# Kernel tuning notes

Measured on AMD Instinct MI355X. Metric: run time of the kernel, lower is better.

The kernel has to match this reference:

```python
import jax, jax.numpy as jnp
import numpy as np

PI_2 = 3.14159 / 2  # matches torch module constant (not exact pi/2, keeps tan finite)
EPS_SUM = 1e-07
EPS_COS = 1e-08  # torch F.cosine_similarity default eps


def setup_inputs() -> dict:
    key = jax.random.key(0)
    k1, k2 = jax.random.split(key)
    B, N, C, H, W = 16, 2000, 512, 7, 7
    # memory is uniform-initialized then sum-normalized per cube, as in __init__
    memory = jax.random.uniform(k1, (N, C, H, W), dtype=jnp.float32)
    memory = memory / (jnp.sum(memory, axis=(1, 2, 3), keepdims=True) + EPS_SUM)
    key_t = jax.random.uniform(k2, (B, C, H, W), dtype=jnp.float32)
    return {"key": key_t, "memory": memory}


def reference(key, memory):
    # _normalize: divide key by its per-sample sum
    k = key / (jnp.sum(key, axis=(1, 2, 3), keepdims=True) + EPS_SUM)
    B = k.shape[0]
    N = memory.shape[0]
    kf = k.reshape(B, -1)            # [B, D], D = C*H*W
    mf = memory.reshape(N, -1)       # [N, D]
    # cosine similarity (torch clamps each norm to eps)
    dots = jnp.einsum('bd,nd->bn', kf, mf)                       # [B, N]
    kn = jnp.maximum(jnp.linalg.norm(kf, axis=-1), EPS_COS)      # [B]
    mn = jnp.maximum(jnp.linalg.norm(mf, axis=-1), EPS_COS)      # [N]
    cos = dots / (kn[:, None] * mn[None, :])
    w = jax.nn.softmax(jnp.tan(cos * PI_2), axis=1)              # [B, N]
    # read: sum over memory cubes weighted by address w
    return jnp.einsum('bn,nchw->bchw', w, memory)                # [B, C, H, W]
```

## Files before the change

kernel.cpp:

```cpp
#include <hip/hip_runtime.h>
#include <math.h>

#define B 16
#define N 2000
#define D 25088
#define D4 6272
#define PI2 1.570795f
#define KC 28
#define KSPAN (D / KC)
#define KTILES (KSPAN / 32)
#define NT (D / 32)
#define NCHUNK 20
#define NPER (N / NCHUNK)
#define SELHI 0x07060302u

typedef __attribute__((ext_vector_type(8))) short short8;
typedef __attribute__((ext_vector_type(4))) float f32x4;
typedef unsigned int uint;

union pk { uint4 u; short8 s; };
__device__ __forceinline__ short8 as_s8(uint4 u) { pk p; p.u = u; return p.s; }

__device__ __forceinline__ float wave_sum(float v) {
#pragma unroll
    for (int off = 32; off > 0; off >>= 1) v += __shfl_xor(v, off, 64);
    return v;
}
__device__ __forceinline__ float wave_max(float v) {
#pragma unroll
    for (int off = 32; off > 0; off >>= 1) v = fmaxf(v, __shfl_xor(v, off, 64));
    return v;
}

__device__ __forceinline__ void cvt_hilo(const float4& a, const float4& b,
                                         short8& hi, short8& lo, float4& msqv) {
    float xs[8] = {a.x, a.y, a.z, a.w, b.x, b.y, b.z, b.w};
    float* mq = &msqv.x;
    uint lu[8];
#pragma unroll
    for (int j = 0; j < 8; ++j) {
        uint u = __float_as_uint(xs[j]);
        float lof = xs[j] - __uint_as_float(u & 0xffff0000u);
        lu[j] = __float_as_uint(lof);
        mq[j & 3] = fmaf(xs[j], xs[j], mq[j & 3]);
    }
    uint4 h, l;
    h.x = __builtin_amdgcn_perm(__float_as_uint(xs[1]), __float_as_uint(xs[0]), SELHI);
    h.y = __builtin_amdgcn_perm(__float_as_uint(xs[3]), __float_as_uint(xs[2]), SELHI);
    h.z = __builtin_amdgcn_perm(__float_as_uint(xs[5]), __float_as_uint(xs[4]), SELHI);
    h.w = __builtin_amdgcn_perm(__float_as_uint(xs[7]), __float_as_uint(xs[6]), SELHI);
    l.x = __builtin_amdgcn_perm(lu[1], lu[0], SELHI);
    l.y = __builtin_amdgcn_perm(lu[3], lu[2], SELHI);
    l.z = __builtin_amdgcn_perm(lu[5], lu[4], SELHI);
    l.w = __builtin_amdgcn_perm(lu[7], lu[6], SELHI);
    hi = as_s8(h); lo = as_s8(l);
}

__global__ void k_split(const float* __restrict__ key, unsigned short* __restrict__ ksw,
                        float* __restrict__ kn2) {
    const int tid  = threadIdx.x;
    const int g    = blockIdx.x * 256 + tid;
    const int tile = g >> 6, lane = g & 63;
    const int m = lane & 15, quad = lane >> 4;
    const float* src = key + (size_t)m * D + tile * 32 + quad * 8;
    float4 x0 = *(const float4*)src;
    float4 x1 = *(const float4*)(src + 4);
    short8 hi, lo;
    float4 msqv = {0.f, 0.f, 0.f, 0.f};
    cvt_hilo(x0, x1, hi, lo, msqv);
    pk ph; ph.s = hi;
    pk pl; pl.s = lo;
    *(uint4*)(ksw + ((size_t)tile * 64 + lane) * 8)        = ph.u;
    *(uint4*)(ksw + ((size_t)(NT + tile) * 64 + lane) * 8) = pl.u;

    float ssq = (msqv.x + msqv.y) + (msqv.z + msqv.w);
    ssq += __shfl_xor(ssq, 16, 64);
    ssq += __shfl_xor(ssq, 32, 64);
    __shared__ float lds[4][16];
    if (quad == 0) lds[tid >> 6][m] = ssq;
    __syncthreads();
    if (tid < 16)
        atomicAdd(&kn2[tid], lds[0][tid] + lds[1][tid] + lds[2][tid] + lds[3][tid]);
}

__global__ __launch_bounds__(256, 3) void k_dots(const float* __restrict__ mem,
                                                 const unsigned short* __restrict__ ksw,
                                                 float* __restrict__ dots,
                                                 float* __restrict__ mn2) {
    const int tid  = threadIdx.x;
    const int lane = tid & 63;
    const int wave = tid >> 6;
    const int n0   = blockIdx.x * 16;
    const int kc   = blockIdx.y * 4 + wave;
    const int nrow = lane & 15, quad = lane >> 4;

    const float4* mrow4 = (const float4*)(mem + (size_t)(n0 + nrow) * D + kc * KSPAN) + quad * 2;
    const uint4* khp = (const uint4*)(ksw + ((size_t)(kc * KTILES) * 64 + lane) * 8);
    const uint4* klp = (const uint4*)(ksw + ((size_t)(NT + kc * KTILES) * 64 + lane) * 8);

    f32x4 ahh = {0.f, 0.f, 0.f, 0.f};
    f32x4 ahl = ahh, alh = ahh;
    float4 msqv = {0.f, 0.f, 0.f, 0.f};

    float4 a0 = mrow4[0], a1 = mrow4[1];
    uint4  ha = khp[0],   la = klp[0];
    float4 b0 = mrow4[8], b1 = mrow4[9];
    uint4  hb = khp[64],  lb = klp[64];

    for (int t = 0; t < KTILES; t += 2) {
        const int t2 = (t + 2 < KTILES) ? t + 2 : t;
        const int t3 = (t + 3 < KTILES) ? t + 3 : t;
        float4 na0 = mrow4[(size_t)t2 * 8], na1 = mrow4[(size_t)t2 * 8 + 1];
        uint4  nha = khp[(size_t)t2 * 64],  nla = klp[(size_t)t2 * 64];
        float4 nb0 = mrow4[(size_t)t3 * 8], nb1 = mrow4[(size_t)t3 * 8 + 1];
        uint4  nhb = khp[(size_t)t3 * 64],  nlb = klp[(size_t)t3 * 64];

        short8 bh, bl;
        cvt_hilo(a0, a1, bh, bl, msqv);
        {
            short8 kh = as_s8(ha), kl = as_s8(la);
            ahh = __builtin_amdgcn_mfma_f32_16x16x32_bf16(kh, bh, ahh, 0, 0, 0);
            ahl = __builtin_amdgcn_mfma_f32_16x16x32_bf16(kh, bl, ahl, 0, 0, 0);
            alh = __builtin_amdgcn_mfma_f32_16x16x32_bf16(kl, bh, alh, 0, 0, 0);
        }
        cvt_hilo(b0, b1, bh, bl, msqv);
        {
            short8 kh = as_s8(hb), kl = as_s8(lb);
            ahh = __builtin_amdgcn_mfma_f32_16x16x32_bf16(kh, bh, ahh, 0, 0, 0);
            ahl = __builtin_amdgcn_mfma_f32_16x16x32_bf16(kh, bl, ahl, 0, 0, 0);
            alh = __builtin_amdgcn_mfma_f32_16x16x32_bf16(kl, bh, alh, 0, 0, 0);
        }
        a0 = na0; a1 = na1; ha = nha; la = nla;
        b0 = nb0; b1 = nb1; hb = nhb; lb = nlb;
    }

#pragma unroll
    for (int r = 0; r < 4; ++r)
        unsafeAtomicAdd(&dots[(size_t)(quad * 4 + r) * N + n0 + nrow],
                        ahh[r] + ahl[r] + alh[r]);

    float msq = (msqv.x + msqv.y) + (msqv.z + msqv.w);
    msq += __shfl_xor(msq, 16, 64);
    msq += __shfl_xor(msq, 32, 64);
    if (quad == 0) unsafeAtomicAdd(&mn2[n0 + nrow], msq);
}

__global__ __launch_bounds__(256, 2) void k_softmax(const float* __restrict__ kn2,
                                                    const float* __restrict__ dots,
                                                    const float* __restrict__ mn2,
                                                    float* __restrict__ w) {
    const int b = blockIdx.x, tid = threadIdx.x;
    const int wv = tid >> 6, ln = tid & 63;
    __shared__ float t[N];
    __shared__ float redB[4], redC[4];

    const float kn = fmaxf(sqrtf(kn2[b]), 1e-8f);

    float mx = -1e30f;
    for (int n = tid; n < N; n += 256) {
        float mn = fmaxf(sqrtf(mn2[n]), 1e-8f);
        float tv = tanf(dots[(size_t)b * N + n] / (kn * mn) * PI2);
        t[n] = tv;
        mx = fmaxf(mx, tv);
    }
    mx = wave_max(mx);
    if (ln == 0) redB[wv] = mx;
    __syncthreads();
    mx = fmaxf(fmaxf(redB[0], redB[1]), fmaxf(redB[2], redB[3]));

    float sum = 0.f;
    for (int n = tid; n < N; n += 256) {
        float e = expf(t[n] - mx);
        t[n] = e;
        sum += e;
    }
    sum = wave_sum(sum);
    if (ln == 0) redC[wv] = sum;
    __syncthreads();
    sum = redC[0] + redC[1] + redC[2] + redC[3];
    const float inv = 1.f / sum;
    for (int n = tid; n < N; n += 256) w[(size_t)b * N + n] = t[n] * inv;
}

__global__ __launch_bounds__(256, 3) void k_out_p(const float4* __restrict__ mem,
                                                  const float* __restrict__ w,
                                                  float4* __restrict__ part) {
    const int tid = threadIdx.x;
    const int d4  = blockIdx.x * 256 + tid;
    const int n0  = blockIdx.y * NPER;

    __shared__ float wt[B * NPER];
    for (int i = tid; i < B * NPER; i += 256)
        wt[i] = w[(size_t)(i / NPER) * N + n0 + (i % NPER)];
    __syncthreads();
    if (d4 >= D4) return;

    const float4* mp = mem + (size_t)n0 * D4 + d4;
    float4 acc[B];
#pragma unroll
    for (int b = 0; b < B; ++b) acc[b] = make_float4(0.f, 0.f, 0.f, 0.f);

    float4 cur[4];
#pragma unroll
    for (int u = 0; u < 4; ++u) cur[u] = mp[(size_t)u * D4];

    for (int g = 0; g < NPER / 4; ++g) {
        const int gn = (g + 1 < NPER / 4) ? g + 1 : g;
        float4 nxt[4];
#pragma unroll
        for (int u = 0; u < 4; ++u) nxt[u] = mp[(size_t)(gn * 4 + u) * D4];
#pragma unroll
        for (int b = 0; b < B; ++b) {
            const float4 wv = *((const float4*)(wt + b * NPER) + g);
            float4 a = acc[b];
            a.x = fmaf(wv.x, cur[0].x, a.x); a.y = fmaf(wv.x, cur[0].y, a.y);
            a.z = fmaf(wv.x, cur[0].z, a.z); a.w = fmaf(wv.x, cur[0].w, a.w);
            a.x = fmaf(wv.y, cur[1].x, a.x); a.y = fmaf(wv.y, cur[1].y, a.y);
            a.z = fmaf(wv.y, cur[1].z, a.z); a.w = fmaf(wv.y, cur[1].w, a.w);
            a.x = fmaf(wv.z, cur[2].x, a.x); a.y = fmaf(wv.z, cur[2].y, a.y);
            a.z = fmaf(wv.z, cur[2].z, a.z); a.w = fmaf(wv.z, cur[2].w, a.w);
            a.x = fmaf(wv.w, cur[3].x, a.x); a.y = fmaf(wv.w, cur[3].y, a.y);
            a.z = fmaf(wv.w, cur[3].z, a.z); a.w = fmaf(wv.w, cur[3].w, a.w);
            acc[b] = a;
        }
#pragma unroll
        for (int u = 0; u < 4; ++u) cur[u] = nxt[u];
    }
#pragma unroll
    for (int b = 0; b < B; ++b)
        part[((size_t)blockIdx.y * B + b) * D4 + d4] = acc[b];
}

__global__ void k_reduce(const float4* __restrict__ part, float4* __restrict__ out) {
    const int i = blockIdx.x * 256 + threadIdx.x;
    float4 s = part[i];
#pragma unroll
    for (int c = 1; c < NCHUNK; ++c) {
        float4 p = part[(size_t)c * B * D4 + i];
        s.x += p.x; s.y += p.y; s.z += p.z; s.w += p.w;
    }
    out[i] = s;
}

__global__ __launch_bounds__(256, 2) void k_out_atomic(const float4* __restrict__ mem,
                                                       const float* __restrict__ w,
                                                       float* __restrict__ out) {
    const int tid = threadIdx.x;
    const int d4  = blockIdx.x * 256 + tid;
    const int n0  = blockIdx.y * NPER;
    __shared__ float wt[B * NPER];
    for (int i = tid; i < B * NPER; i += 256)
        wt[i] = w[(size_t)(i / NPER) * N + n0 + (i % NPER)];
    __syncthreads();
    if (d4 >= D4) return;
    const float4* mp = mem + (size_t)n0 * D4 + d4;
    float4 acc[B];
#pragma unroll
    for (int b = 0; b < B; ++b) acc[b] = make_float4(0.f, 0.f, 0.f, 0.f);
    for (int n = 0; n < NPER; n += 4) {
        float4 mv[4];
#pragma unroll
        for (int u = 0; u < 4; ++u) mv[u] = mp[(size_t)(n + u) * D4];
#pragma unroll
        for (int b = 0; b < B; ++b) {
            float4 a = acc[b];
#pragma unroll
            for (int u = 0; u < 4; ++u) {
                const float wv = wt[b * NPER + n + u];
                a.x = fmaf(wv, mv[u].x, a.x); a.y = fmaf(wv, mv[u].y, a.y);
                a.z = fmaf(wv, mv[u].z, a.z); a.w = fmaf(wv, mv[u].w, a.w);
            }
            acc[b] = a;
        }
    }
#pragma unroll
    for (int b = 0; b < B; ++b) {
        float* op = out + (size_t)b * D + (size_t)d4 * 4;
        unsafeAtomicAdd(op + 0, acc[b].x);
        unsafeAtomicAdd(op + 1, acc[b].y);
        unsafeAtomicAdd(op + 2, acc[b].z);
        unsafeAtomicAdd(op + 3, acc[b].w);
    }
}

extern "C" void kernel_launch(void* const* d_in, const int* in_sizes, int n_in,
                              void* d_out, int out_size, void* d_ws, size_t ws_size,
                              hipStream_t stream) {
    const float* key = (const float*)d_in[0];
    const float* mem = (const float*)d_in[1];
    float* out = (float*)d_out;

    float* ws = (float*)d_ws;
    unsigned short* ksw = (unsigned short*)ws;
    float* dots  = ws + 401408;
    float* mn2   = dots + (size_t)B * N;
    float* kn2   = mn2 + N;
    float* w     = kn2 + 16;
    float* part  = w + (size_t)B * N;
    const size_t need_full =
        (size_t)(401408 + B * N + N + 16 + B * N + (size_t)NCHUNK * B * D) * 4;

    hipMemsetAsync(dots, 0, (size_t)(B * N + N + 16) * sizeof(float), stream);
    k_split<<<dim3(NT * 64 / 256), 256, 0, stream>>>(key, ksw, kn2);
    k_dots<<<dim3(N / 16, KC / 4), 256, 0, stream>>>(mem, ksw, dots, mn2);
    k_softmax<<<dim3(B), 256, 0, stream>>>(kn2, dots, mn2, w);
    if (ws_size >= need_full) {
        k_out_p<<<dim3((D4 + 255) / 256, NCHUNK), 256, 0, stream>>>((const float4*)mem, w, (float4*)part);
        k_reduce<<<dim3(B * D4 / 256), 256, 0, stream>>>((const float4*)part, (float4*)out);
    } else {
        hipMemsetAsync(d_out, 0, (size_t)B * D * sizeof(float), stream);
        k_out_atomic<<<dim3((D4 + 255) / 256, NCHUNK), 256, 0, stream>>>((const float4*)mem, w, out);
    }
}
```

Before: 336.4 us.

## Store partial output sums as scaled fp16 and fold memset into split kernel

The partial sums of the output read are scaled by 2^20 and stored as fp16 instead of fp32, which halves the write and read traffic of the partial buffer between k_out_p and k_reduce. The separate memset is removed: k_split now zeroes the dots and mn2 buffers itself. Key norms are written as per-block partials and summed inside the softmax kernel rather than with atomics. k_out_p's launch bounds are also raised to four blocks per SM. The fp16 partials lose precision and may overflow or underflow depending on how large the weighted sums are, which could push the output past the reference tolerance.

```diff
diff --git a/kernel.cpp b/kernel.cpp
--- a/kernel.cpp
+++ b/kernel.cpp
@@ -1,4 +1,5 @@
 #include <hip/hip_runtime.h>
+#include <hip/hip_fp16.h>
 #include <math.h>
 
 #define B 16
@@ -10,9 +11,12 @@
 #define KSPAN (D / KC)
 #define KTILES (KSPAN / 32)
 #define NT (D / 32)
+#define KBLK (NT / 4)
 #define NCHUNK 20
 #define NPER (N / NCHUNK)
 #define SELHI 0x07060302u
+#define PSCALE 1048576.0f
+#define PINV   (1.0f / 1048576.0f)
 
 typedef __attribute__((ext_vector_type(8))) short short8;
 typedef __attribute__((ext_vector_type(4))) float f32x4;
@@ -20,6 +24,7 @@
 
 union pk { uint4 u; short8 s; };
 __device__ __forceinline__ short8 as_s8(uint4 u) { pk p; p.u = u; return p.s; }
+union hpk { __half2 h; uint u; };
 
 __device__ __forceinline__ float wave_sum(float v) {
 #pragma unroll
@@ -57,9 +62,11 @@
 }
 
 __global__ void k_split(const float* __restrict__ key, unsigned short* __restrict__ ksw,
-                        float* __restrict__ kn2) {
+                        float* __restrict__ zdst, float* __restrict__ kpart) {
     const int tid  = threadIdx.x;
-    const int g    = blockIdx.x * 256 + tid;
+    const int bx   = blockIdx.x;
+    const int g    = bx * 256 + tid;
+    if (g < B * N + N) zdst[g] = 0.f;
     const int tile = g >> 6, lane = g & 63;
     const int m = lane & 15, quad = lane >> 4;
     const float* src = key + (size_t)m * D + tile * 32 + quad * 8;
@@ -80,7 +87,7 @@
     if (quad == 0) lds[tid >> 6][m] = ssq;
     __syncthreads();
     if (tid < 16)
-        atomicAdd(&kn2[tid], lds[0][tid] + lds[1][tid] + lds[2][tid] + lds[3][tid]);
+        kpart[bx * 16 + tid] = lds[0][tid] + lds[1][tid] + lds[2][tid] + lds[3][tid];
 }
 
 __global__ __launch_bounds__(256, 3) void k_dots(const float* __restrict__ mem,
@@ -145,7 +152,7 @@
     if (quad == 0) unsafeAtomicAdd(&mn2[n0 + nrow], msq);
 }
 
-__global__ __launch_bounds__(256, 2) void k_softmax(const float* __restrict__ kn2,
+__global__ __launch_bounds__(256, 2) void k_softmax(const float* __restrict__ kpart,
                                                     const float* __restrict__ dots,
                                                     const float* __restrict__ mn2,
                                                     float* __restrict__ w) {
@@ -154,7 +161,12 @@
     __shared__ float t[N];
     __shared__ float redB[4], redC[4];
 
-    const float kn = fmaxf(sqrtf(kn2[b]), 1e-8f);
+    float s = (tid < KBLK) ? kpart[tid * 16 + b] : 0.f;
+    s = wave_sum(s);
+    if (ln == 0) redB[wv] = s;
+    __syncthreads();
+    const float kn = fmaxf(sqrtf(redB[0] + redB[1] + redB[2] + redB[3]), 1e-8f);
+    __syncthreads();
 
     float mx = -1e30f;
     for (int n = tid; n < N; n += 256) {
@@ -182,9 +194,9 @@
     for (int n = tid; n < N; n += 256) w[(size_t)b * N + n] = t[n] * inv;
 }
 
-__global__ __launch_bounds__(256, 3) void k_out_p(const float4* __restrict__ mem,
+__global__ __launch_bounds__(256, 4) void k_out_p(const float4* __restrict__ mem,
                                                   const float* __restrict__ w,
-                                                  float4* __restrict__ part) {
+                                                  uint2* __restrict__ part) {
     const int tid = threadIdx.x;
     const int d4  = blockIdx.x * 256 + tid;
     const int n0  = blockIdx.y * NPER;
@@ -227,19 +239,26 @@
         for (int u = 0; u < 4; ++u) cur[u] = nxt[u];
     }
 #pragma unroll
-    for (int b = 0; b < B; ++b)
-        part[((size_t)blockIdx.y * B + b) * D4 + d4] = acc[b];
-}
-
-__global__ void k_reduce(const float4* __restrict__ part, float4* __restrict__ out) {
+    for (int b = 0; b < B; ++b) {
+        hpk p0, p1;
+        p0.h = __floats2half2_rn(acc[b].x * PSCALE, acc[b].y * PSCALE);
+        p1.h = __floats2half2_rn(acc[b].z * PSCALE, acc[b].w * PSCALE);
+        uint2 v; v.x = p0.u; v.y = p1.u;
+        part[((size_t)blockIdx.y * B + b) * D4 + d4] = v;
+    }
+}
+
+__global__ void k_reduce(const uint2* __restrict__ part, float4* __restrict__ out) {
     const int i = blockIdx.x * 256 + threadIdx.x;
-    float4 s = part[i];
-#pragma unroll
-    for (int c = 1; c < NCHUNK; ++c) {
-        float4 p = part[(size_t)c * B * D4 + i];
-        s.x += p.x; s.y += p.y; s.z += p.z; s.w += p.w;
-    }
-    out[i] = s;
+    float sx = 0.f, sy = 0.f, sz = 0.f, sw = 0.f;
+#pragma unroll
+    for (int c = 0; c < NCHUNK; ++c) {
+        uint2 v = part[(size_t)c * B * D4 + i];
+        hpk a, b2; a.u = v.x; b2.u = v.y;
+        float2 f0 = __half22float2(a.h), f1 = __half22float2(b2.h);
+        sx += f0.x; sy += f0.y; sz += f1.x; sw += f1.y;
+    }
+    out[i] = make_float4(sx * PINV, sy * PINV, sz * PINV, sw * PINV);
 }
 
 __global__ __launch_bounds__(256, 2) void k_out_atomic(const float4* __restrict__ mem,
@@ -294,19 +313,18 @@
     unsigned short* ksw = (unsigned short*)ws;
     float* dots  = ws + 401408;
     float* mn2   = dots + (size_t)B * N;
-    float* kn2   = mn2 + N;
-    float* w     = kn2 + 16;
+    float* kpart = mn2 + N;
+    float* w     = kpart + (size_t)KBLK * 16;
     float* part  = w + (size_t)B * N;
     const size_t need_full =
-        (size_t)(401408 + B * N + N + 16 + B * N + (size_t)NCHUNK * B * D) * 4;
-
-    hipMemsetAsync(dots, 0, (size_t)(B * N + N + 16) * sizeof(float), stream);
-    k_split<<<dim3(NT * 64 / 256), 256, 0, stream>>>(key, ksw, kn2);
+        (size_t)(401408 + B * N + N + KBLK * 16 + B * N + (size_t)NCHUNK * B * D4 * 2) * 4;
+
+    k_split<<<dim3(KBLK), 256, 0, stream>>>(key, ksw, dots, kpart);
     k_dots<<<dim3(N / 16, KC / 4), 256, 0, stream>>>(mem, ksw, dots, mn2);
-    k_softmax<<<dim3(B), 256, 0, stream>>>(kn2, dots, mn2, w);
+    k_softmax<<<dim3(B), 256, 0, stream>>>(kpart, dots, mn2, w);
     if (ws_size >= need_full) {
-        k_out_p<<<dim3((D4 + 255) / 256, NCHUNK), 256, 0, stream>>>((const float4*)mem, w, (float4*)part);
-        k_reduce<<<dim3(B * D4 / 256), 256, 0, stream>>>((const float4*)part, (float4*)out);
+        k_out_p<<<dim3((D4 + 255) / 256, NCHUNK), 256, 0, stream>>>((const float4*)mem, w, (uint2*)part);
+        k_reduce<<<dim3(B * D4 / 256), 256, 0, stream>>>((const uint2*)part, (float4*)out);
     } else {
         hipMemsetAsync(d_out, 0, (size_t)B * D * sizeof(float), stream);
         k_out_atomic<<<dim3((D4 + 255) / 256, NCHUNK), 256, 0, stream>>>((const float4*)mem, w, out);
```

Result: no change. 332.4 us (-1.2%).
